# Kernel tuning notes

Measured on AMD Instinct MI355X. Metric: run time of the kernel, lower is better.

The kernel has to match this reference:

```python
import jax, jax.numpy as jnp
import numpy as np

B, S, D, P = 8, 2048, 1024, 32
H = 8
HD = D // H  # head_dim = 128


def setup_inputs() -> dict:
    key = jax.random.key(0)
    ks = jax.random.split(key, 14)
    x = jax.random.normal(ks[0], (B, S, D), dtype=jnp.float32)
    # 8 trigram projections, each Linear(D, HD, bias=False): stacked (H, HD, D)
    W_proj = jax.random.normal(ks[1], (H, HD, D), dtype=jnp.float32) * 0.02
    # resonance frequencies, init randn * 0.01 as in source
    freqs = jax.random.normal(ks[2], (H, HD), dtype=jnp.float32) * 0.01
    # per-head polarity generators Linear(HD, P) + Tanh
    Wp = jax.random.normal(ks[3], (H, P, HD), dtype=jnp.float32) * (1.0 / np.sqrt(HD))
    bp = jnp.zeros((H, P), dtype=jnp.float32)
    # impedance modulator: Linear(1,16) -> GELU -> Linear(16,1) -> Softplus
    w1 = jax.random.normal(ks[4], (16,), dtype=jnp.float32)
    b1 = jnp.zeros((16,), dtype=jnp.float32)
    w2 = jax.random.normal(ks[5], (16,), dtype=jnp.float32) * 0.25
    b2 = jnp.zeros((), dtype=jnp.float32)
    # output projection Linear(D, D) and LayerNorm(D)
    Wo = jax.random.normal(ks[6], (D, D), dtype=jnp.float32) * 0.02
    bo = jnp.zeros((D,), dtype=jnp.float32)
    ln_g = jnp.ones((D,), dtype=jnp.float32)
    ln_b = jnp.zeros((D,), dtype=jnp.float32)
    return {"x": x, "W_proj": W_proj, "freqs": freqs, "Wp": Wp, "bp": bp,
            "w1": w1, "b1": b1, "w2": w2, "b2": b2,
            "Wo": Wo, "bo": bo, "ln_g": ln_g, "ln_b": ln_b}


def reference(x, W_proj, freqs, Wp, bp, w1, b1, w2, b2, Wo, bo, ln_g, ln_b):
    # heads[i] = (x @ W_i^T) * cos(pi * freqs[i])  -> (B, H, S, HD)
    heads = jnp.einsum('bsd,hed->bhse', x, W_proj)
    heads = heads * jnp.cos(freqs * jnp.pi)[None, :, None, :]

    # --- GuaXiangDuiChong: impedance matrix (B, H, H) ---
    hm = heads.mean(axis=2)                                   # (B, H, HD)
    pv = jnp.tanh(jnp.einsum('bhd,hpd->bhp', hm, Wp) + bp[None])
    nrm = jnp.maximum(jnp.linalg.norm(pv, axis=-1, keepdims=True), 1e-12)
    pm = pv / nrm                                             # F.normalize
    dp = jnp.einsum('bip,bjp->bij', pm, pm)                   # (B, H, H)
    h1 = jax.nn.gelu(dp[..., None] * w1 + b1, approximate=False)  # (B,H,H,16)
    imp = jax.nn.softplus(jnp.einsum('bijk,k->bij', h1, w2) + b2)
    eye = jnp.eye(H, dtype=jnp.float32)
    impedance = imp * (1.0 - eye)[None]                       # zero diagonal

    # --- cross-head transfer with fused causal scaling ---
    # Original builds (B,S,S,HD) then masked mean over keys; mathematically
    # this equals scaling transfer[b,s,:] by (s+1)/S.
    coef = jnp.where(eye[None].astype(bool), 0.0, 0.1 / (1.0 + impedance))
    scale = (jnp.arange(S, dtype=jnp.float32) + 1.0) / S      # causal mean factor
    transfer = jnp.einsum('bij,bjse->bise', coef, heads) * scale[None, None, :, None]
    out_heads = heads + transfer                              # (B, H, S, HD)

    merged = out_heads.transpose(0, 2, 1, 3).reshape(B, S, D)
    y = merged @ Wo.T + bo + x                                # dropout = 0
    mu = y.mean(axis=-1, keepdims=True)
    var = ((y - mu) ** 2).mean(axis=-1, keepdims=True)
    y = (y - mu) * jax.lax.rsqrt(var + 1e-5) * ln_g + ln_b
    return y
```

## Files before the change

kernel.cpp:

```cpp
#include <hip/hip_runtime.h>
#include <hip/hip_bf16.h>

#define B_  8
#define S_  2048
#define D_  1024
#define H_  8
#define HD_ 128
#define P_  32
#define BS_ (B_*S_)
#define PI_F 3.14159265358979323846f

typedef unsigned short u16;
typedef unsigned int u32;
typedef __attribute__((ext_vector_type(4))) float  f32x4;
typedef __attribute__((ext_vector_type(8))) __bf16 bf16x8;
typedef __attribute__((ext_vector_type(8))) unsigned short u16x8;

__device__ __forceinline__ u16 f2b(float f) {
  __hip_bfloat16 h = __float2bfloat16(f);
  return __builtin_bit_cast(u16, h);
}
__device__ __forceinline__ float b2f(u16 b) {
  return __bfloat162float(__builtin_bit_cast(__hip_bfloat16, b));
}

__device__ __forceinline__ void gload_lds16(const void* g, void* l) {
  auto gp = (const __attribute__((address_space(1))) unsigned int*)g;
  auto lp = (__attribute__((address_space(3))) unsigned int*)l;
  __builtin_amdgcn_global_load_lds(gp, lp, 16, 0, 0);
}

#define FENCE() asm volatile("" ::: "memory")
#define BAR() do { FENCE(); __builtin_amdgcn_sched_barrier(0); \
                   __builtin_amdgcn_s_barrier(); \
                   __builtin_amdgcn_sched_barrier(0); FENCE(); } while (0)
#define LGKM0() do { asm volatile("s_waitcnt lgkmcnt(0)" ::: "memory"); \
                     __builtin_amdgcn_sched_barrier(0); } while (0)
#define VMC(N) do { asm volatile("s_waitcnt vmcnt(" #N ")" ::: "memory"); \
                    __builtin_amdgcn_sched_barrier(0); } while (0)

__global__ __launch_bounds__(256) void cvt_x_kernel(const float* __restrict__ x,
                                                    u16* __restrict__ xb,
                                                    float* __restrict__ xsum) {
  const int r0 = blockIdx.x * 32;
  const int b = r0 >> 11;
  const int c = threadIdx.x * 4;
  float s0 = 0.f, s1 = 0.f, s2 = 0.f, s3 = 0.f;
#pragma unroll 4
  for (int i = 0; i < 32; ++i) {
    const float4 v = *reinterpret_cast<const float4*>(x + (size_t)(r0 + i) * D_ + c);
    ushort4 o;
    o.x = f2b(v.x); o.y = f2b(v.y); o.z = f2b(v.z); o.w = f2b(v.w);
    *reinterpret_cast<ushort4*>(xb + (size_t)(r0 + i) * D_ + c) = o;
    s0 += v.x; s1 += v.y; s2 += v.z; s3 += v.w;
  }
  atomicAdd(&xsum[b * D_ + c + 0], s0);
  atomicAdd(&xsum[b * D_ + c + 1], s1);
  atomicAdd(&xsum[b * D_ + c + 2], s2);
  atomicAdd(&xsum[b * D_ + c + 3], s3);
}

__global__ __launch_bounds__(256) void cvt_w_kernel(const float* __restrict__ Wproj,
                                                    const float* __restrict__ freqs,
                                                    const float* __restrict__ Wo,
                                                    u16* __restrict__ Wt1,
                                                    u16* __restrict__ Wob) {
  int i = blockIdx.x * blockDim.x + threadIdx.x;
  const int total = D_ * D_;
  for (; i < total; i += gridDim.x * blockDim.x) {
    int n = i >> 10;
    float c = cosf(PI_F * freqs[n]);
    Wt1[i] = f2b(Wproj[i] * c);
    Wob[i] = f2b(Wo[i]);
  }
}

__global__ __launch_bounds__(512, 2) void gemm8p(const u16* __restrict__ A,
                                                 const u16* __restrict__ Bm,
                                                 u16* __restrict__ C,
                                                 int M, int N, int K) {
  extern __shared__ __align__(16) u16 smem[];
  const int tid = threadIdx.x;
  const int l = tid & 63;
  const int wid = tid >> 6;
  const int wm = wid >> 2, wn = wid & 3;
  const int lr = l & 15, lg = l >> 4;
  const int bm0 = blockIdx.x * 256, bn0 = blockIdx.y * 256;

  const int srow = tid >> 3;
  const int scol = ((tid & 7) ^ (srow & 7)) * 8;

  f32x4 acc[8][4] = {};
  bf16x8 af[4][2], b0[2][2], b1[2][2];

  u16* const As = smem;
  u16* const Bs = smem + 32768;

  auto stageA = [&](int half, int kt, int buf) {
    const u16* src = A + (size_t)(bm0 + half * 128 + srow) * K + kt * 64 + scol;
    u16* dst = As + buf * 16384 + half * 8192 + tid * 8;
    gload_lds16(src, dst);
    gload_lds16(src + (size_t)64 * K, dst + 4096);
  };
  auto stageB = [&](int half, int kt, int buf) {
    const u16* src = Bm + (size_t)(bn0 + half * 128 + srow) * K + kt * 64 + scol;
    u16* dst = Bs + buf * 16384 + half * 8192 + tid * 8;
    gload_lds16(src, dst);
    gload_lds16(src + (size_t)64 * K, dst + 4096);
  };
  auto readA = [&](int buf, int mh) {
#pragma unroll
    for (int mi = 0; mi < 4; ++mi)
#pragma unroll
      for (int kk = 0; kk < 2; ++kk) {
        int r = wm * 128 + mh * 64 + mi * 16 + lr;
        int g = (kk * 4 + lg) ^ (lr & 7);
        af[mi][kk] = *reinterpret_cast<const bf16x8*>(As + buf * 16384 + r * 64 + g * 8);
      }
  };
  auto readB = [&](bf16x8 (&bb)[2][2], int buf, int nh) {
#pragma unroll
    for (int ni = 0; ni < 2; ++ni)
#pragma unroll
      for (int kk = 0; kk < 2; ++kk) {
        int r = wn * 64 + (nh * 2 + ni) * 16 + lr;
        int g = (kk * 4 + lg) ^ (lr & 7);
        bb[ni][kk] = *reinterpret_cast<const bf16x8*>(Bs + buf * 16384 + r * 64 + g * 8);
      }
  };
  auto mmaq = [&](int mh, int nh, bf16x8 (&bb)[2][2]) {
    __builtin_amdgcn_s_setprio(1);
#pragma unroll
    for (int mi = 0; mi < 4; ++mi)
#pragma unroll
      for (int ni = 0; ni < 2; ++ni)
#pragma unroll
        for (int kk = 0; kk < 2; ++kk)
          acc[mh * 4 + mi][nh * 2 + ni] = __builtin_amdgcn_mfma_f32_16x16x32_bf16(
              af[mi][kk], bb[ni][kk], acc[mh * 4 + mi][nh * 2 + ni], 0, 0, 0);
    __builtin_amdgcn_s_setprio(0);
  };

  const int NT = K >> 6;

  stageA(0, 0, 0); stageB(0, 0, 0); stageA(1, 0, 0); stageB(1, 0, 0);
  stageA(0, 1, 1); stageB(0, 1, 1); stageA(1, 1, 1);
  VMC(6); BAR();

  auto tile = [&](int u, int buf) {
    readA(buf, 0); readB(b0, buf, 0);
    if (u + 1 < NT) stageB(1, u + 1, buf ^ 1);
    BAR(); LGKM0();
    mmaq(0, 0, b0);
    BAR();
    readB(b1, buf, 1);
    BAR(); LGKM0();
    mmaq(0, 1, b1);
    BAR();
    readA(buf, 1);
    if (u + 2 < NT) stageB(0, u + 2, buf);
    BAR(); LGKM0();
    mmaq(1, 0, b0);
    BAR();
    if (u + 2 < NT) { stageA(0, u + 2, buf); stageA(1, u + 2, buf); }
    BAR(); LGKM0();
    mmaq(1, 1, b1);
    if (u + 1 < NT) {
      if (u + 2 < NT) { VMC(6); } else { VMC(0); }
    }
    BAR();
  };

  for (int u = 0; u < NT; u += 2) {
    tile(u, 0);
    tile(u + 1, 1);
  }

  const int jr = (l >> 4) * 4;
#pragma unroll
  for (int h = 0; h < 2; ++h) {
    __syncthreads();
    if (wm == h) {
#pragma unroll
      for (int m = 0; m < 8; ++m)
#pragma unroll
        for (int n = 0; n < 4; ++n)
#pragma unroll
          for (int j = 0; j < 4; ++j)
            smem[(m * 16 + jr + j) * 256 + wn * 64 + n * 16 + lr] = f2b(acc[m][n][j]);
    }
    __syncthreads();
#pragma unroll
    for (int i = 0; i < 8; ++i) {
      int g = tid + i * 512;
      int r = g >> 5, cg = g & 31;
      *reinterpret_cast<u16x8*>(C + (size_t)(bm0 + h * 128 + r) * N + bn0 + cg * 8) =
          *reinterpret_cast<const u16x8*>(smem + g * 8);
    }
  }
}

__global__ __launch_bounds__(256) void hm_gemv(const float* __restrict__ xsum,
                                               const u16* __restrict__ Wt1,
                                               float* __restrict__ hm) {
  const int gw = blockIdx.x * 4 + (threadIdx.x >> 6);
  const int b = gw >> 10, d = gw & 1023;
  const int lane = threadIdx.x & 63;
  const u16* wr = Wt1 + (size_t)d * D_ + lane * 16;
  const float* xs = xsum + b * D_ + lane * 16;
  u16x8 w0 = *reinterpret_cast<const u16x8*>(wr);
  u16x8 w1 = *reinterpret_cast<const u16x8*>(wr + 8);
  float4 x0 = reinterpret_cast<const float4*>(xs)[0];
  float4 x1 = reinterpret_cast<const float4*>(xs)[1];
  float4 x2 = reinterpret_cast<const float4*>(xs)[2];
  float4 x3 = reinterpret_cast<const float4*>(xs)[3];
  float s = 0.f;
  const float* xf = (const float*)&x0;
#pragma unroll
  for (int k = 0; k < 8; ++k) s += xf[k] * b2f(w0[k]);
  const float* xg = (const float*)&x2;
#pragma unroll
  for (int k = 0; k < 8; ++k) s += xg[k] * b2f(w1[k]);
  (void)x1; (void)x3;
#pragma unroll
  for (int off = 32; off; off >>= 1) s += __shfl_xor(s, off);
  if (lane == 0) hm[gw] = s * (1.0f / S_);
}

__global__ __launch_bounds__(256) void coef2_kernel(const float* __restrict__ hm,
                                                    const float* __restrict__ Wp,
                                                    const float* __restrict__ bp,
                                                    const float* __restrict__ w1,
                                                    const float* __restrict__ b1,
                                                    const float* __restrict__ w2,
                                                    const float* __restrict__ b2,
                                                    float* __restrict__ coef) {
  __shared__ float hm_s[D_];
  __shared__ float pm_s[H_ * P_];
  const int b = blockIdx.x, t = threadIdx.x;
#pragma unroll
  for (int q = 0; q < 4; ++q) hm_s[t * 4 + q] = hm[b * D_ + t * 4 + q];
  __syncthreads();
  {
    const int h = t >> 5, p = t & 31;
    float a = bp[h * P_ + p];
    const float* wp = Wp + (size_t)(h * P_ + p) * HD_;
#pragma unroll 4
    for (int e = 0; e < HD_; ++e) a += hm_s[h * HD_ + e] * wp[e];
    pm_s[t] = tanhf(a);
  }
  __syncthreads();
  if (t < 8) {
    float ss = 0.f;
    for (int p = 0; p < P_; ++p) { float v = pm_s[t * P_ + p]; ss += v * v; }
    float inv = 1.0f / fmaxf(sqrtf(ss), 1e-12f);
    for (int p = 0; p < P_; ++p) pm_s[t * P_ + p] *= inv;
  }
  __syncthreads();
  if (t < 64) {
    const int i = t >> 3, j = t & 7;
    float dp = 0.f;
    for (int p = 0; p < P_; ++p)
      dp += pm_s[i * P_ + p] * pm_s[j * P_ + p];
    float acc = b2[0];
#pragma unroll
    for (int k = 0; k < 16; ++k) {
      float z = dp * w1[k] + b1[k];
      float g = 0.5f * z * (1.0f + erff(z * 0.70710678118654752f));
      acc += g * w2[k];
    }
    float sp = (acc > 20.f) ? acc : log1pf(expf(acc));
    coef[b * 64 + t] = (i == j) ? 0.f : 0.1f / (1.0f + sp);
  }
}

__global__ __launch_bounds__(256) void mix_kernel(const u16* __restrict__ heads,
                                                  const float* __restrict__ coef,
                                                  u16* __restrict__ mixed) {
  __shared__ float cfs[64];
  const int r = blockIdx.x * 4 + (threadIdx.x >> 6);
  const int b = blockIdx.x >> 9;
  const int s = r & 2047;
  const int t = threadIdx.x & 63;
  if (threadIdx.x < 64) cfs[threadIdx.x] = coef[b * 64 + threadIdx.x];
  __syncthreads();
  const u16* hp = heads + (size_t)r * D_ + 2 * t;
  float hx[8], hy[8];
#pragma unroll
  for (int j = 0; j < 8; ++j) {
    u32 v = *reinterpret_cast<const u32*>(hp + j * 128);
    hx[j] = b2f((u16)(v & 0xffff));
    hy[j] = b2f((u16)(v >> 16));
  }
  const float scale = (float)(s + 1) * (1.0f / S_);
  u16* op = mixed + (size_t)r * D_ + 2 * t;
#pragma unroll
  for (int i = 0; i < 8; ++i) {
    float tx = 0.f, ty = 0.f;
#pragma unroll
    for (int j = 0; j < 8; ++j) {
      float c = cfs[i * 8 + j];
      tx += c * hx[j]; ty += c * hy[j];
    }
    u32 o = (u32)f2b(hx[i] + scale * tx) | ((u32)f2b(hy[i] + scale * ty) << 16);
    *reinterpret_cast<u32*>(op + i * 128) = o;
  }
}

__global__ __launch_bounds__(256) void ln_kernel(const u16* __restrict__ ypre,
                                                 const float* __restrict__ x,
                                                 const float* __restrict__ bo,
                                                 const float* __restrict__ g,
                                                 const float* __restrict__ be,
                                                 float* __restrict__ out) {
  const int r = blockIdx.x, t = threadIdx.x;
  const u16* yp = ypre + (size_t)r * D_;
  const float* xp = x + (size_t)r * D_;
  const int d0 = t * 4;
  float4 xv = reinterpret_cast<const float4*>(xp)[t];
  ushort4 yv = reinterpret_cast<const ushort4*>(yp)[t];
  float v[4];
  float s = 0.f, ss = 0.f;
#pragma unroll
  for (int q = 0; q < 4; ++q) {
    float y = b2f(((u16*)&yv)[q]) + bo[d0 + q] + ((const float*)&xv)[q];
    v[q] = y; s += y; ss += y * y;
  }
#pragma unroll
  for (int off = 32; off; off >>= 1) {
    s += __shfl_xor(s, off);
    ss += __shfl_xor(ss, off);
  }
  __shared__ float rs[4], rss[4];
  int w = t >> 6;
  if ((t & 63) == 0) { rs[w] = s; rss[w] = ss; }
  __syncthreads();
  s = rs[0] + rs[1] + rs[2] + rs[3];
  ss = rss[0] + rss[1] + rss[2] + rss[3];
  float mu = s * (1.0f / D_);
  float var = ss * (1.0f / D_) - mu * mu;
  float rstd = rsqrtf(var + 1e-5f);
  float4 ov;
#pragma unroll
  for (int q = 0; q < 4; ++q)
    ((float*)&ov)[q] = (v[q] - mu) * rstd * g[d0 + q] + be[d0 + q];
  reinterpret_cast<float4*>(out + (size_t)r * D_)[t] = ov;
}

extern "C" void kernel_launch(void* const* d_in, const int* in_sizes, int n_in,
                              void* d_out, int out_size, void* d_ws, size_t ws_size,
                              hipStream_t stream) {
  (void)in_sizes; (void)n_in; (void)out_size; (void)ws_size;
  const float* x     = (const float*)d_in[0];
  const float* Wproj = (const float*)d_in[1];
  const float* freqs = (const float*)d_in[2];
  const float* Wp    = (const float*)d_in[3];
  const float* bp    = (const float*)d_in[4];
  const float* w1    = (const float*)d_in[5];
  const float* b1    = (const float*)d_in[6];
  const float* w2    = (const float*)d_in[7];
  const float* b2    = (const float*)d_in[8];
  const float* Wo    = (const float*)d_in[9];
  const float* bo    = (const float*)d_in[10];
  const float* ln_g  = (const float*)d_in[11];
  const float* ln_b  = (const float*)d_in[12];
  float* out = (float*)d_out;

  char* ws = (char*)d_ws;
  u16*   xbf   = (u16*)ws;
  u16*   heads = (u16*)(ws + 33554432);
  u16*   Wt1   = (u16*)(ws + 67108864);
  u16*   Wob   = (u16*)(ws + 69206016);
  float* xsum  = (float*)(ws + 71303168);
  float* hm    = (float*)(ws + 71335936);
  float* coef  = (float*)(ws + 71368704);

  hipFuncSetAttribute((const void*)gemm8p,
                      hipFuncAttributeMaxDynamicSharedMemorySize, 131072);

  hipMemsetAsync(xsum, 0, B_ * D_ * sizeof(float), stream);

  cvt_x_kernel<<<512, 256, 0, stream>>>(x, xbf, xsum);
  cvt_w_kernel<<<1024, 256, 0, stream>>>(Wproj, freqs, Wo, Wt1, Wob);

  hm_gemv<<<2048, 256, 0, stream>>>(xsum, Wt1, hm);
  coef2_kernel<<<8, 256, 0, stream>>>(hm, Wp, bp, w1, b1, w2, b2, coef);

  dim3 g1(BS_ / 256, D_ / 256);
  gemm8p<<<g1, 512, 131072, stream>>>(xbf, Wt1, heads, BS_, D_, D_);

  mix_kernel<<<BS_ / 4, 256, 0, stream>>>(heads, coef, xbf );

  gemm8p<<<g1, 512, 131072, stream>>>(xbf, Wob, heads , BS_, D_, D_);

  ln_kernel<<<BS_, 256, 0, stream>>>(heads, x, bo, ln_g, ln_b, out);
}
```

Measured before the change: 267.5 us.

## Restructure GEMM main loop barriers, swizzle epilogue, read bf16 residual in LayerNorm

The GEMM tile loop is reordered so each half-tile issues all LDS fragment reads and then two MFMA groups, with fewer block barriers and no explicit lgkmcnt waits. Global prefetch stages are interleaved differently. The epilogue now writes the whole 256x256 tile to LDS in one pass using an XOR-swizzled column layout to avoid bank conflicts, then stores it out after a single barrier. LayerNorm reads the residual from the bf16 copy of x instead of fp32, halving that read, and the mix output gets its own buffer so xbf is kept. The trade-off is lower residual precision, plus reliance on compiler-inserted LDS waits, which may be less well placed.

```diff
diff --git a/kernel.cpp b/kernel.cpp
--- a/kernel.cpp
+++ b/kernel.cpp
@@ -34,8 +34,6 @@
 #define BAR() do { FENCE(); __builtin_amdgcn_sched_barrier(0); \
                    __builtin_amdgcn_s_barrier(); \
                    __builtin_amdgcn_sched_barrier(0); FENCE(); } while (0)
-#define LGKM0() do { asm volatile("s_waitcnt lgkmcnt(0)" ::: "memory"); \
-                     __builtin_amdgcn_sched_barrier(0); } while (0)
 #define VMC(N) do { asm volatile("s_waitcnt vmcnt(" #N ")" ::: "memory"); \
                     __builtin_amdgcn_sched_barrier(0); } while (0)
 
@@ -143,31 +141,26 @@
 
   const int NT = K >> 6;
 
-  stageA(0, 0, 0); stageB(0, 0, 0); stageA(1, 0, 0); stageB(1, 0, 0);
-  stageA(0, 1, 1); stageB(0, 1, 1); stageA(1, 1, 1);
+  stageB(0, 0, 0); stageB(1, 0, 0); stageA(0, 0, 0); stageA(1, 0, 0);
+  stageB(0, 1, 1); stageA(0, 1, 1); stageA(1, 1, 1);
   VMC(6); BAR();
 
   auto tile = [&](int u, int buf) {
-    readA(buf, 0); readB(b0, buf, 0);
     if (u + 1 < NT) stageB(1, u + 1, buf ^ 1);
-    BAR(); LGKM0();
+    readA(buf, 0);
+    readB(b0, buf, 0);
+    readB(b1, buf, 1);
     mmaq(0, 0, b0);
-    BAR();
-    readB(b1, buf, 1);
-    BAR(); LGKM0();
     mmaq(0, 1, b1);
     BAR();
+    if (u + 2 < NT) { stageB(0, u + 2, buf); stageA(0, u + 2, buf); }
     readA(buf, 1);
-    if (u + 2 < NT) stageB(0, u + 2, buf);
-    BAR(); LGKM0();
     mmaq(1, 0, b0);
+    mmaq(1, 1, b1);
     BAR();
-    if (u + 2 < NT) { stageA(0, u + 2, buf); stageA(1, u + 2, buf); }
-    BAR(); LGKM0();
-    mmaq(1, 1, b1);
-    if (u + 1 < NT) {
-      if (u + 2 < NT) { VMC(6); } else { VMC(0); }
-    }
+    if (u + 2 < NT) stageA(1, u + 2, buf);
+    if (u + 2 < NT)      { VMC(6); }
+    else if (u + 1 < NT) { VMC(0); }
     BAR();
   };
 
@@ -176,27 +169,25 @@
     tile(u + 1, 1);
   }
 
-  const int jr = (l >> 4) * 4;
-#pragma unroll
-  for (int h = 0; h < 2; ++h) {
-    __syncthreads();
-    if (wm == h) {
-#pragma unroll
-      for (int m = 0; m < 8; ++m)
-#pragma unroll
-        for (int n = 0; n < 4; ++n)
-#pragma unroll
-          for (int j = 0; j < 4; ++j)
-            smem[(m * 16 + jr + j) * 256 + wn * 64 + n * 16 + lr] = f2b(acc[m][n][j]);
-    }
-    __syncthreads();
-#pragma unroll
-    for (int i = 0; i < 8; ++i) {
-      int g = tid + i * 512;
-      int r = g >> 5, cg = g & 31;
-      *reinterpret_cast<u16x8*>(C + (size_t)(bm0 + h * 128 + r) * N + bn0 + cg * 8) =
-          *reinterpret_cast<const u16x8*>(smem + g * 8);
-    }
+  const int jr = lg * 4;
+#pragma unroll
+  for (int m = 0; m < 8; ++m)
+#pragma unroll
+    for (int n = 0; n < 4; ++n)
+#pragma unroll
+      for (int j = 0; j < 4; ++j) {
+        int row = wm * 128 + m * 16 + jr + j;
+        int cin = ((n * 16 + lr) ^ (lg << 4));
+        smem[row * 256 + wn * 64 + cin] = f2b(acc[m][n][j]);
+      }
+  BAR();
+#pragma unroll
+  for (int i = 0; i < 16; ++i) {
+    int g = tid + i * 512;
+    int r = g >> 5, c8 = (g & 31) * 8;
+    int src = r * 256 + (c8 & ~63) + ((c8 & 63) ^ (((r >> 2) & 3) << 4));
+    *reinterpret_cast<u16x8*>(C + (size_t)(bm0 + r) * N + bn0 + c8) =
+        *reinterpret_cast<const u16x8*>(smem + src);
   }
 }
 
@@ -308,22 +299,22 @@
 }
 
 __global__ __launch_bounds__(256) void ln_kernel(const u16* __restrict__ ypre,
-                                                 const float* __restrict__ x,
+                                                 const u16* __restrict__ xb,
                                                  const float* __restrict__ bo,
                                                  const float* __restrict__ g,
                                                  const float* __restrict__ be,
                                                  float* __restrict__ out) {
   const int r = blockIdx.x, t = threadIdx.x;
   const u16* yp = ypre + (size_t)r * D_;
-  const float* xp = x + (size_t)r * D_;
+  const u16* xp = xb + (size_t)r * D_;
   const int d0 = t * 4;
-  float4 xv = reinterpret_cast<const float4*>(xp)[t];
+  ushort4 xv = reinterpret_cast<const ushort4*>(xp)[t];
   ushort4 yv = reinterpret_cast<const ushort4*>(yp)[t];
   float v[4];
   float s = 0.f, ss = 0.f;
 #pragma unroll
   for (int q = 0; q < 4; ++q) {
-    float y = b2f(((u16*)&yv)[q]) + bo[d0 + q] + ((const float*)&xv)[q];
+    float y = b2f(((u16*)&yv)[q]) + bo[d0 + q] + b2f(((u16*)&xv)[q]);
     v[q] = y; s += y; ss += y * y;
   }
 #pragma unroll
@@ -369,11 +360,12 @@
   char* ws = (char*)d_ws;
   u16*   xbf   = (u16*)ws;
   u16*   heads = (u16*)(ws + 33554432);
-  u16*   Wt1   = (u16*)(ws + 67108864);
-  u16*   Wob   = (u16*)(ws + 69206016);
-  float* xsum  = (float*)(ws + 71303168);
-  float* hm    = (float*)(ws + 71335936);
-  float* coef  = (float*)(ws + 71368704);
+  u16*   mixed = (u16*)(ws + 67108864);
+  u16*   Wt1   = (u16*)(ws + 100663296);
+  u16*   Wob   = (u16*)(ws + 102760448);
+  float* xsum  = (float*)(ws + 104857600);
+  float* hm    = (float*)(ws + 104890368);
+  float* coef  = (float*)(ws + 104923136);
 
   hipFuncSetAttribute((const void*)gemm8p,
                       hipFuncAttributeMaxDynamicSharedMemorySize, 131072);
@@ -389,9 +381,9 @@
   dim3 g1(BS_ / 256, D_ / 256);
   gemm8p<<<g1, 512, 131072, stream>>>(xbf, Wt1, heads, BS_, D_, D_);
 
-  mix_kernel<<<BS_ / 4, 256, 0, stream>>>(heads, coef, xbf );
-
-  gemm8p<<<g1, 512, 131072, stream>>>(xbf, Wob, heads , BS_, D_, D_);
-
-  ln_kernel<<<BS_, 256, 0, stream>>>(heads, x, bo, ln_g, ln_b, out);
-}
+  mix_kernel<<<BS_ / 4, 256, 0, stream>>>(heads, coef, mixed);
+
+  gemm8p<<<g1, 512, 131072, stream>>>(mixed, Wob, heads , BS_, D_, D_);
+
+  ln_kernel<<<BS_, 256, 0, stream>>>(heads, xbf, bo, ln_g, ln_b, out);
+}
```

After: 270.9 us. No clear change (+1.3%).
